# Optimization experiments

Measured on AMD Instinct MI355X. Metric: run time of the kernel, lower is better.

The kernel has to match this reference:

```python
import jax, jax.numpy as jnp
import numpy as np

EPS = 1e-5

def setup_inputs() -> dict:
    key = jax.random.key(0)
    ks = jax.random.split(key, 12)
    B, L, d_model, d_pair = 2, 384, 1024, 128
    h = jax.random.normal(ks[0], (B, L, d_model), dtype=jnp.float32)
    # torch.nn.Linear params: W [out,in], b [out]
    Wi = jax.random.normal(ks[1], (d_pair, d_model), dtype=jnp.float32) * 0.02
    bi = jnp.zeros((d_pair,), dtype=jnp.float32)
    Wj = jax.random.normal(ks[2], (d_pair, d_model), dtype=jnp.float32) * 0.02
    bj = jnp.zeros((d_pair,), dtype=jnp.float32)
    bilinear_weight = jax.random.normal(ks[3], (d_pair, d_pair, d_pair), dtype=jnp.float32) * 0.02
    gamma = jnp.ones((d_pair,), dtype=jnp.float32)
    beta = jnp.zeros((d_pair,), dtype=jnp.float32)
    mix_w = jax.random.normal(ks[4], (d_pair, d_pair, 3, 3), dtype=jnp.float32) * 0.02  # OIHW
    out_w = jax.random.normal(ks[5], (d_pair, d_pair, 1, 1), dtype=jnp.float32) * 0.05
    out_b = jnp.zeros((d_pair,), dtype=jnp.float32)
    return {"h": h, "Wi": Wi, "bi": bi, "Wj": Wj, "bj": bj,
            "bilinear_weight": bilinear_weight, "gamma": gamma, "beta": beta,
            "mix_w": mix_w, "out_w": out_w, "out_b": out_b}

def _instance_norm(x, gamma, beta):
    # x: [B, C, H, W]; normalize per (b, c) over spatial dims
    mean = jnp.mean(x, axis=(2, 3), keepdims=True)
    var = jnp.var(x, axis=(2, 3), keepdims=True)
    xn = (x - mean) * jax.lax.rsqrt(var + EPS)
    return xn * gamma[None, :, None, None] + beta[None, :, None, None]

def _conv(x, w):
    return jax.lax.conv_general_dilated(
        x, w, window_strides=(1, 1), padding='SAME',
        dimension_numbers=('NCHW', 'OIHW', 'NCHW'))

def reference(h, Wi, bi, Wj, bj, bilinear_weight, gamma, beta, mix_w, out_w, out_b):
    ui = h @ Wi.T + bi  # [B, L, d_pair]
    vj = h @ Wj.T + bj  # [B, L, d_pair]
    # pairwise bilinear: [B, d_pair(k), L, L]
    feat = jnp.einsum('bli,ijk,bmj->bklm', ui, bilinear_weight, vj)
    feat = _instance_norm(feat, gamma, beta)
    feat = jax.nn.relu(feat)
    feat = jax.nn.relu(_conv(feat, mix_w))
    return _conv(feat, out_w) + out_b[None, :, None, None]
```

## Files before the change

kernel.cpp:

```cpp
#include <hip/hip_runtime.h>
#include <hip/hip_bf16.h>
#include <stdint.h>

typedef __bf16 bf16_t;
typedef __bf16 bf16x8 __attribute__((ext_vector_type(8)));
typedef float  f32x4  __attribute__((ext_vector_type(4)));

#define MFMA(a, b, c) __builtin_amdgcn_mfma_f32_16x16x32_bf16((a), (b), (c), 0, 0, 0)

__device__ __forceinline__ void gload_lds16(const void* g, void* l) {
  __builtin_amdgcn_global_load_lds(
      (const __attribute__((address_space(1))) unsigned int*)(g),
      (__attribute__((address_space(3))) unsigned int*)(l), 16, 0, 0);
}

__global__ __launch_bounds__(128) void k_linear(
    const float* __restrict__ h, const float* __restrict__ Wi,
    const float* __restrict__ bi, const float* __restrict__ Wj,
    const float* __restrict__ bj, bf16_t* __restrict__ ui,
    bf16_t* __restrict__ vj) {
  int bl = blockIdx.x;
  int which = blockIdx.y;
  const float* W = which ? Wj : Wi;
  const float* bias = which ? bj : bi;
  bf16_t* out = which ? vj : ui;
  __shared__ float hrow[1024];
  for (int i = threadIdx.x; i < 1024; i += 128) hrow[i] = h[bl * 1024 + i];
  __syncthreads();
  int p = threadIdx.x;
  const float* w = W + (size_t)p * 1024;
  float acc = bias[p];
  for (int i = 0; i < 1024; i += 4) {
    f32x4 wv = *(const f32x4*)(w + i);
    acc += hrow[i] * wv[0] + hrow[i + 1] * wv[1] + hrow[i + 2] * wv[2] +
           hrow[i + 3] * wv[3];
  }
  out[bl * 128 + p] = (bf16_t)acc;
}

__global__ __launch_bounds__(256) void k_wt(const float* __restrict__ W,
                                            bf16_t* __restrict__ Wt) {
  int j = blockIdx.x;
  int i0 = blockIdx.y * 32, k0 = blockIdx.z * 32;
  __shared__ float tile[32][33];
  int tx = threadIdx.x & 31, ty = threadIdx.x >> 5;
#pragma unroll
  for (int r = 0; r < 4; r++) {
    int ii = ty + r * 8;
    tile[ii][tx] = W[(size_t)(i0 + ii) * 16384 + j * 128 + (k0 + tx)];
  }
  __syncthreads();
#pragma unroll
  for (int r = 0; r < 4; r++) {
    int kk = ty + r * 8;
    Wt[(size_t)(k0 + kk) * 16384 + j * 128 + (i0 + tx)] = (bf16_t)tile[tx][kk];
  }
}

__global__ __launch_bounds__(256) void k_wc(const float* __restrict__ mw,
                                            bf16_t* __restrict__ Wc2) {
  int idx = blockIdx.x * 256 + threadIdx.x;
  if (idx < 147456) {
    int e = idx & 7, ln = (idx >> 3) & 63, fm = (idx >> 9) & 3;
    int kc = (idx >> 11) & 3, wrh = (idx >> 13) & 1, tap = idx >> 14;
    int oc = wrh * 64 + fm * 16 + (ln & 15);
    int ic = kc * 32 + (ln >> 4) * 8 + e;
    Wc2[idx] = (bf16_t)mw[oc * 1152 + ic * 9 + tap];
  }
}

__global__ __launch_bounds__(256) void k_wo(const float* __restrict__ ow,
                                            bf16_t* __restrict__ Wo2) {
  int idx = blockIdx.x * 256 + threadIdx.x;
  if (idx < 16384) {
    int e = idx & 7, ln = (idx >> 3) & 63, fm = (idx >> 9) & 3;
    int kc = (idx >> 11) & 3, wrh = (idx >> 13) & 1;
    int oc2 = wrh * 64 + fm * 16 + (ln & 15);
    int mc = kc * 32 + (ln >> 4) * 8 + e;
    Wo2[idx] = (bf16_t)ow[oc2 * 128 + mc];
  }
}

__global__ __launch_bounds__(256) void k_tgemm(const bf16_t* __restrict__ A,
                                               const bf16_t* __restrict__ Bt,
                                               bf16_t* __restrict__ T) {
  int m0 = blockIdx.x * 64;
  int n0 = blockIdx.y * 64;
  __shared__ bf16_t Al[64][136], Bl[64][136];
  for (int c = threadIdx.x; c < 64 * 16; c += 256) {
    int row = c >> 4, col = (c & 15) * 8;
    *(uint4*)&Al[row][col] = *(const uint4*)&A[(size_t)(m0 + row) * 128 + col];
    *(uint4*)&Bl[row][col] = *(const uint4*)&Bt[(size_t)(n0 + row) * 128 + col];
  }
  __syncthreads();
  int w = threadIdx.x >> 6, ln = threadIdx.x & 63;
  int wr = (w >> 1) * 32, wc = (w & 1) * 32;
  int lr = ln & 15, hi8 = (ln >> 4) * 8, rb = (ln >> 4) * 4;
  f32x4 acc[2][2] = {};
#pragma unroll
  for (int kc = 0; kc < 128; kc += 32) {
    bf16x8 a0 = *(bf16x8*)&Al[wr + lr][kc + hi8];
    bf16x8 a1 = *(bf16x8*)&Al[wr + 16 + lr][kc + hi8];
    bf16x8 b0 = *(bf16x8*)&Bl[wc + lr][kc + hi8];
    bf16x8 b1 = *(bf16x8*)&Bl[wc + 16 + lr][kc + hi8];
    acc[0][0] = MFMA(a0, b0, acc[0][0]);
    acc[0][1] = MFMA(a0, b1, acc[0][1]);
    acc[1][0] = MFMA(a1, b0, acc[1][0]);
    acc[1][1] = MFMA(a1, b1, acc[1][1]);
  }
#pragma unroll
  for (int fm = 0; fm < 2; fm++)
#pragma unroll
    for (int fn = 0; fn < 2; fn++) {
      int col = n0 + wc + fn * 16 + lr;
#pragma unroll
      for (int r = 0; r < 4; r++) {
        int row = m0 + wr + fm * 16 + rb + r;
        T[(size_t)row * 16384 + col] = (bf16_t)acc[fm][fn][r];
      }
    }
}

__global__ __launch_bounds__(256) void k_feat(const bf16_t* __restrict__ T,
                                              const bf16_t* __restrict__ Vb,
                                              bf16_t* __restrict__ F,
                                              float* __restrict__ part) {
  int bl = blockIdx.x;
  int b = bl / 384;
  __shared__ __align__(16) char sm[52224];
  bf16_t (*Tl)[136] = (bf16_t(*)[136])(sm);
  bf16_t (*Fb)[136] = (bf16_t(*)[136])(sm + 34816);
  float* rs = (float*)(sm);
  float* rq = (float*)(sm + 8192);
  const bf16_t* tsrc = T + (size_t)bl * 16384;
  for (int c = threadIdx.x; c < 128 * 16; c += 256) {
    int row = c >> 4, col = (c & 15) * 8;
    *(uint4*)&Tl[row][col] = *(const uint4*)&tsrc[row * 128 + col];
  }
  __syncthreads();
  int w = threadIdx.x >> 6, ln = threadIdx.x & 63;
  int wr = (w >> 1) * 64, wc = (w & 1) * 32;
  int lr = ln & 15, g = ln >> 4, hi8 = g * 8, rb = g * 4;
  size_t base = (size_t)bl * 384 * 128;
  float s8[8] = {}, q8[8] = {};
  int col8 = threadIdx.x & 15;
  for (int mt = 0; mt < 6; mt++) {
    bf16x8 vf[2][4];
#pragma unroll
    for (int fn = 0; fn < 2; fn++)
#pragma unroll
      for (int kc = 0; kc < 4; kc++) {
        int m = mt * 64 + wc + fn * 16 + lr;
        vf[fn][kc] = *(const bf16x8*)&Vb[(size_t)(b * 384 + m) * 128 +
                                         kc * 32 + hi8];
      }
    f32x4 acc[4][2] = {};
#pragma unroll
    for (int kc = 0; kc < 4; kc++) {
#pragma unroll
      for (int fm = 0; fm < 4; fm++) {
        bf16x8 av = *(bf16x8*)&Tl[wr + fm * 16 + lr][kc * 32 + hi8];
        acc[fm][0] = MFMA(av, vf[0][kc], acc[fm][0]);
        acc[fm][1] = MFMA(av, vf[1][kc], acc[fm][1]);
      }
    }
    __syncthreads();
    union {
      bf16_t h[4];
      uint2 u;
    } pk;
#pragma unroll
    for (int fm = 0; fm < 4; fm++)
#pragma unroll
      for (int fn = 0; fn < 2; fn++) {
        int m = wc + fn * 16 + lr;
        int kb = wr + fm * 16 + rb;
#pragma unroll
        for (int r = 0; r < 4; r++) pk.h[r] = (bf16_t)acc[fm][fn][r];
        *(uint2*)&Fb[m][kb] = pk.u;
      }
    __syncthreads();
    for (int c = threadIdx.x; c < 64 * 16; c += 256) {
      int row = c >> 4;
      uint4 v = *(uint4*)&Fb[row][col8 * 8];
      *(uint4*)&F[base + (size_t)(mt * 64 + row) * 128 + col8 * 8] = v;
      const bf16_t* hp = (const bf16_t*)&v;
#pragma unroll
      for (int e = 0; e < 8; e++) {
        float f = (float)hp[e];
        s8[e] += f;
        q8[e] += f * f;
      }
    }
  }
  int sub = threadIdx.x >> 4;
#pragma unroll
  for (int e = 0; e < 8; e++) {
    rs[(sub * 16 + col8) * 8 + e] = s8[e];
    rq[(sub * 16 + col8) * 8 + e] = q8[e];
  }
  __syncthreads();
  if (threadIdx.x < 128) {
    int k = threadIdx.x, kg = k >> 3, e = k & 7;
    float S = 0.f, Q = 0.f;
#pragma unroll
    for (int s = 0; s < 16; s++) {
      S += rs[(s * 16 + kg) * 8 + e];
      Q += rq[(s * 16 + kg) * 8 + e];
    }
    part[(size_t)bl * 256 + k] = S;
    part[(size_t)bl * 256 + 128 + k] = Q;
  }
}

__global__ __launch_bounds__(64) void k_stats2(const float* __restrict__ part,
                                               const float* __restrict__ gamma,
                                               const float* __restrict__ beta,
                                               float* __restrict__ ss) {
  int k = blockIdx.x, b = blockIdx.y, t = threadIdx.x;
  float S = 0.f, Q = 0.f;
  for (int l = t; l < 384; l += 64) {
    S += part[(size_t)(b * 384 + l) * 256 + k];
    Q += part[(size_t)(b * 384 + l) * 256 + 128 + k];
  }
#pragma unroll
  for (int o = 32; o; o >>= 1) {
    S += __shfl_down(S, o, 64);
    Q += __shfl_down(Q, o, 64);
  }
  if (t == 0) {
    const float inv = 1.0f / 147456.0f;
    float mean = S * inv;
    float var = Q * inv - mean * mean;
    float sc = gamma[k] * rsqrtf(var + 1e-5f);
    ss[b * 256 + k] = sc;
    ss[b * 256 + 128 + k] = beta[k] - mean * sc;
  }
}

__global__ __launch_bounds__(256, 2) void k_conv(
    const bf16_t* __restrict__ Fn, const float* __restrict__ ss,
    const bf16_t* __restrict__ Wc2, const bf16_t* __restrict__ Wo2,
    const float* __restrict__ outb, float* __restrict__ out) {
  int orig = blockIdx.x;
  int wg = (orig & 7) * 288 + (orig >> 3);
  int xt = wg % 3;
  int t1 = wg / 3;
  int b = t1 / 384;
  int y = t1 - b * 384;
  int x0 = xt * 128;

  __shared__ __align__(16) char sm[66048];
  char* smB = sm + 32768;

  int tid = threadIdx.x;
  int w = tid >> 6, ln = tid & 63;
  int wrh = w >> 1, pxb = (w & 1) * 64;
  int lr = ln & 15, g = ln >> 4, rb = g * 4;

  int c8 = (tid & 15) * 8;
  float scr[8], shr[8];
  {
    const float* sb = ss + b * 256;
    *(f32x4*)&scr[0] = *(const f32x4*)&sb[c8];
    *(f32x4*)&scr[4] = *(const f32x4*)&sb[c8 + 4];
    *(f32x4*)&shr[0] = *(const f32x4*)&sb[128 + c8];
    *(f32x4*)&shr[4] = *(const f32x4*)&sb[128 + c8 + 4];
  }

  f32x4 acc[4][4] = {};
  for (int dy = 0; dy < 3; dy++) {
    int yy = y + dy - 1;
    bool yok = (yy >= 0 && yy < 384);
    __syncthreads();
    const char* Frow = (const char*)Fn + (size_t)(b * 384 + yy) * 98304;
#pragma unroll
    for (int i = 0; i < 9; i++) {
      int s = tid + i * 256;
      if (s < 2080) {
        int px = s >> 4, c16 = (s & 15) << 4;
        int xx = x0 - 1 + px;
        bf16x8 o;
        if (yok && xx >= 0 && xx < 384) {
          bf16x8 f = *(const bf16x8*)(Frow + (size_t)xx * 256 + c16);
#pragma unroll
          for (int e = 0; e < 8; e++) {
            float v = (float)f[e] * scr[e] + shr[e];
            o[e] = (bf16_t)(v > 0.f ? v : 0.f);
          }
        } else {
#pragma unroll
          for (int e = 0; e < 8; e++) o[e] = (bf16_t)0.f;
        }
        int byte = (px << 8) + c16;
        *(bf16x8*)(smB + (byte ^ ((px & 7) << 4))) = o;
      }
    }
#pragma unroll
    for (int dx = 0; dx < 3; dx++) {
      if (dx) __syncthreads();
      const char* WcTap = (const char*)Wc2 + (size_t)(dy * 3 + dx) * 32768;
#pragma unroll
      for (int i = 0; i < 8; i++) {
        int o4 = w * 8192 + i * 1024 + ln * 16;
        gload_lds16(WcTap + o4, sm + o4);
      }
      __syncthreads();
#pragma unroll
      for (int kc = 0; kc < 4; kc++) {
        bf16x8 av[4], bv[4];
#pragma unroll
        for (int fn = 0; fn < 4; fn++) {
          int row = pxb + fn * 16 + lr + dx;
          int byte = (row << 8) + (kc << 6) + (g << 4);
          bv[fn] = *(const bf16x8*)(smB + (byte ^ ((row & 7) << 4)));
        }
#pragma unroll
        for (int fm = 0; fm < 4; fm++)
          av[fm] = *(const bf16x8*)(sm + wrh * 16384 + kc * 4096 + fm * 1024 +
                                    ln * 16);
#pragma unroll
        for (int fm = 0; fm < 4; fm++)
#pragma unroll
          for (int fn = 0; fn < 4; fn++)
            acc[fm][fn] = MFMA(av[fm], bv[fn], acc[fm][fn]);
      }
    }
  }
  __syncthreads();
#pragma unroll
  for (int i = 0; i < 8; i++) {
    int o4 = w * 8192 + i * 1024 + ln * 16;
    gload_lds16((const char*)Wo2 + o4, sm + o4);
  }
  union {
    bf16_t hh[4];
    uint2 u;
  } pk;
#pragma unroll
  for (int fm = 0; fm < 4; fm++)
#pragma unroll
    for (int fn = 0; fn < 4; fn++) {
      int px = pxb + fn * 16 + lr;
      int mcb = wrh * 64 + fm * 16 + rb;
#pragma unroll
      for (int r = 0; r < 4; r++) {
        float v = acc[fm][fn][r];
        pk.hh[r] = (bf16_t)(v > 0.f ? v : 0.f);
      }
      int byte = (px << 8) + (mcb << 1);
      *(uint2*)(smB + (byte ^ ((px & 7) << 4))) = pk.u;
    }
  __syncthreads();
  f32x4 acc2[4][4] = {};
#pragma unroll
  for (int kc = 0; kc < 4; kc++) {
    bf16x8 av[4], bv[4];
#pragma unroll
    for (int fn = 0; fn < 4; fn++) {
      int row = pxb + fn * 16 + lr;
      int byte = (row << 8) + (kc << 6) + (g << 4);
      bv[fn] = *(const bf16x8*)(smB + (byte ^ ((row & 7) << 4)));
    }
#pragma unroll
    for (int fm = 0; fm < 4; fm++)
      av[fm] = *(const bf16x8*)(sm + wrh * 16384 + kc * 4096 + fm * 1024 +
                                ln * 16);
#pragma unroll
    for (int fm = 0; fm < 4; fm++)
#pragma unroll
      for (int fn = 0; fn < 4; fn++)
        acc2[fm][fn] = MFMA(av[fm], bv[fn], acc2[fm][fn]);
  }
  f32x4 obv[4];
#pragma unroll
  for (int fm = 0; fm < 4; fm++)
    obv[fm] = *(const f32x4*)&outb[wrh * 64 + fm * 16 + rb];
#pragma unroll
  for (int fm = 0; fm < 4; fm++)
#pragma unroll
    for (int fn = 0; fn < 4; fn++) {
      int x = x0 + pxb + fn * 16 + lr;
#pragma unroll
      for (int r = 0; r < 4; r++) {
        int oc2 = wrh * 64 + fm * 16 + rb + r;
        out[((size_t)(b * 128 + oc2) * 384 + y) * 384 + x] =
            acc2[fm][fn][r] + obv[fm][r];
      }
    }
}

extern "C" void kernel_launch(void* const* d_in, const int* in_sizes, int n_in,
                              void* d_out, int out_size, void* d_ws,
                              size_t ws_size, hipStream_t stream) {
  const float* h = (const float*)d_in[0];
  const float* Wi = (const float*)d_in[1];
  const float* bi = (const float*)d_in[2];
  const float* Wj = (const float*)d_in[3];
  const float* bj = (const float*)d_in[4];
  const float* Wbl = (const float*)d_in[5];
  const float* gamma = (const float*)d_in[6];
  const float* beta = (const float*)d_in[7];
  const float* mw = (const float*)d_in[8];
  const float* ow = (const float*)d_in[9];
  const float* ob = (const float*)d_in[10];
  float* out = (float*)d_out;

  char* ws = (char*)d_ws;
  size_t off = 0;
  auto alloc = [&](size_t bytes) -> void* {
    void* p = ws + off;
    off = (off + bytes + 255) & ~(size_t)255;
    return p;
  };
  bf16_t* ui_b = (bf16_t*)alloc(768 * 128 * 2);
  bf16_t* vj_b = (bf16_t*)alloc(768 * 128 * 2);
  bf16_t* Wt = (bf16_t*)alloc((size_t)2097152 * 2);
  bf16_t* Wc2 = (bf16_t*)alloc((size_t)147456 * 2);
  bf16_t* Wo2 = (bf16_t*)alloc((size_t)16384 * 2);
  bf16_t* T = (bf16_t*)alloc((size_t)768 * 16384 * 2);
  bf16_t* F = (bf16_t*)alloc((size_t)2 * 384 * 384 * 128 * 2);
  float* part = (float*)alloc((size_t)768 * 256 * 4);
  float* ssb = (float*)alloc((size_t)2 * 256 * 4);

  k_linear<<<dim3(768, 2), 128, 0, stream>>>(h, Wi, bi, Wj, bj, ui_b, vj_b);
  k_wt<<<dim3(128, 4, 4), 256, 0, stream>>>(Wbl, Wt);
  k_wc<<<(147456 + 255) / 256, 256, 0, stream>>>(mw, Wc2);
  k_wo<<<64, 256, 0, stream>>>(ow, Wo2);
  k_tgemm<<<dim3(12, 256), 256, 0, stream>>>(ui_b, Wt, T);
  k_feat<<<768, 256, 0, stream>>>(T, vj_b, F, part);
  k_stats2<<<dim3(128, 2), 64, 0, stream>>>(part, gamma, beta, ssb);
  k_conv<<<2304, 256, 0, stream>>>(F, ssb, Wc2, Wo2, ob, out);
}
```

Measured before the change: 258.6 us.

## Rewrite input projection as bf16 MFMA GEMM and raise MFMA wave priority in conv

Replaces the per-row scalar fp32 linear kernel with a tiled bf16 MFMA GEMM. Each 256-thread block computes a 64-row tile of ui or vj, staging h and W through LDS in bf16. The old kernel had every block re-read the full weight matrix from global memory, and the new one is meant to cut that traffic and the scalar FMA work. It also wraps the MFMA loops of the conv kernel in s_setprio so waves doing matrix math get scheduling priority. The bf16 conversion of h and W before the GEMM adds rounding error. The new GEMM launches only 24 blocks, which underuses the GPU.

```diff
diff --git a/kernel.cpp b/kernel.cpp
--- a/kernel.cpp
+++ b/kernel.cpp
@@ -14,28 +14,73 @@
       (__attribute__((address_space(3))) unsigned int*)(l), 16, 0, 0);
 }
 
-__global__ __launch_bounds__(128) void k_linear(
+__global__ __launch_bounds__(256) void k_lin2(
     const float* __restrict__ h, const float* __restrict__ Wi,
     const float* __restrict__ bi, const float* __restrict__ Wj,
     const float* __restrict__ bj, bf16_t* __restrict__ ui,
     bf16_t* __restrict__ vj) {
-  int bl = blockIdx.x;
+  int m0 = blockIdx.x * 64;
   int which = blockIdx.y;
   const float* W = which ? Wj : Wi;
   const float* bias = which ? bj : bi;
   bf16_t* out = which ? vj : ui;
-  __shared__ float hrow[1024];
-  for (int i = threadIdx.x; i < 1024; i += 128) hrow[i] = h[bl * 1024 + i];
-  __syncthreads();
-  int p = threadIdx.x;
-  const float* w = W + (size_t)p * 1024;
-  float acc = bias[p];
-  for (int i = 0; i < 1024; i += 4) {
-    f32x4 wv = *(const f32x4*)(w + i);
-    acc += hrow[i] * wv[0] + hrow[i + 1] * wv[1] + hrow[i + 2] * wv[2] +
-           hrow[i + 3] * wv[3];
-  }
-  out[bl * 128 + p] = (bf16_t)acc;
+  __shared__ bf16_t Al[64][136];
+  __shared__ bf16_t Bl[128][136];
+  int w = threadIdx.x >> 6, ln = threadIdx.x & 63;
+  int wr = (w >> 1) * 32, wc = (w & 1) * 64;
+  int lr = ln & 15, hi8 = (ln >> 4) * 8, rb = (ln >> 4) * 4;
+  f32x4 acc[2][4] = {};
+  for (int kc0 = 0; kc0 < 1024; kc0 += 128) {
+    __syncthreads();
+    for (int c = threadIdx.x; c < 64 * 16; c += 256) {
+      int row = c >> 4, col = (c & 15) * 8;
+      const float* src = &h[(size_t)(m0 + row) * 1024 + kc0 + col];
+      f32x4 a = *(const f32x4*)src, b2 = *(const f32x4*)(src + 4);
+      bf16x8 o;
+#pragma unroll
+      for (int e = 0; e < 4; e++) {
+        o[e] = (bf16_t)a[e];
+        o[e + 4] = (bf16_t)b2[e];
+      }
+      *(bf16x8*)&Al[row][col] = o;
+    }
+    for (int c = threadIdx.x; c < 128 * 16; c += 256) {
+      int row = c >> 4, col = (c & 15) * 8;
+      const float* src = &W[(size_t)row * 1024 + kc0 + col];
+      f32x4 a = *(const f32x4*)src, b2 = *(const f32x4*)(src + 4);
+      bf16x8 o;
+#pragma unroll
+      for (int e = 0; e < 4; e++) {
+        o[e] = (bf16_t)a[e];
+        o[e + 4] = (bf16_t)b2[e];
+      }
+      *(bf16x8*)&Bl[row][col] = o;
+    }
+    __syncthreads();
+#pragma unroll
+    for (int kc = 0; kc < 128; kc += 32) {
+      bf16x8 a0 = *(bf16x8*)&Al[wr + lr][kc + hi8];
+      bf16x8 a1 = *(bf16x8*)&Al[wr + 16 + lr][kc + hi8];
+#pragma unroll
+      for (int fn = 0; fn < 4; fn++) {
+        bf16x8 bv = *(bf16x8*)&Bl[wc + fn * 16 + lr][kc + hi8];
+        acc[0][fn] = MFMA(a0, bv, acc[0][fn]);
+        acc[1][fn] = MFMA(a1, bv, acc[1][fn]);
+      }
+    }
+  }
+#pragma unroll
+  for (int fm = 0; fm < 2; fm++)
+#pragma unroll
+    for (int fn = 0; fn < 4; fn++) {
+      int col = wc + fn * 16 + lr;
+      float bb = bias[col];
+#pragma unroll
+      for (int r = 0; r < 4; r++) {
+        int row = m0 + wr + fm * 16 + rb + r;
+        out[row * 128 + col] = (bf16_t)(acc[fm][fn][r] + bb);
+      }
+    }
 }
 
 __global__ __launch_bounds__(256) void k_wt(const float* __restrict__ W,
@@ -306,6 +351,7 @@
         gload_lds16(WcTap + o4, sm + o4);
       }
       __syncthreads();
+      __builtin_amdgcn_s_setprio(1);
 #pragma unroll
       for (int kc = 0; kc < 4; kc++) {
         bf16x8 av[4], bv[4];
@@ -325,6 +371,7 @@
           for (int fn = 0; fn < 4; fn++)
             acc[fm][fn] = MFMA(av[fm], bv[fn], acc[fm][fn]);
       }
+      __builtin_amdgcn_s_setprio(0);
     }
   }
   __syncthreads();
@@ -353,6 +400,7 @@
     }
   __syncthreads();
   f32x4 acc2[4][4] = {};
+  __builtin_amdgcn_s_setprio(1);
 #pragma unroll
   for (int kc = 0; kc < 4; kc++) {
     bf16x8 av[4], bv[4];
@@ -372,6 +420,7 @@
       for (int fn = 0; fn < 4; fn++)
         acc2[fm][fn] = MFMA(av[fm], bv[fn], acc2[fm][fn]);
   }
+  __builtin_amdgcn_s_setprio(0);
   f32x4 obv[4];
 #pragma unroll
   for (int fm = 0; fm < 4; fm++)
@@ -423,7 +472,7 @@
   float* part = (float*)alloc((size_t)768 * 256 * 4);
   float* ssb = (float*)alloc((size_t)2 * 256 * 4);
 
-  k_linear<<<dim3(768, 2), 128, 0, stream>>>(h, Wi, bi, Wj, bj, ui_b, vj_b);
+  k_lin2<<<dim3(12, 2), 256, 0, stream>>>(h, Wi, bi, Wj, bj, ui_b, vj_b);
   k_wt<<<dim3(128, 4, 4), 256, 0, stream>>>(Wbl, Wt);
   k_wc<<<(147456 + 255) / 256, 256, 0, stream>>>(mw, Wc2);
   k_wo<<<64, 256, 0, stream>>>(ow, Wo2);
```

Measured after the change: 210.7 us. -18.5%, faster.
